# Kernel optimization log

Measured on AMD Instinct MI355X. Metric: run time of the kernel, lower is better.

Reference implementation:

```python
import jax, jax.numpy as jnp
import numpy as np

P, C_IN, C_OUT, V = 3, 64, 32, 8192
EPS = 1e-5


def _layernorm(z, w, b):
    # normalized_shape = [C, 1, V]: normalize jointly over channel/temporal/node dims
    m = jnp.mean(z, axis=(1, 2, 3), keepdims=True)
    v = jnp.var(z, axis=(1, 2, 3), keepdims=True)
    return (z - m) * jax.lax.rsqrt(v + EPS) * w + b


def setup_inputs() -> dict:
    key = jax.random.key(0)
    ks = jax.random.split(key, 8)
    return {
        "x": jax.random.normal(ks[0], (1, C_IN, 1, V), jnp.float32),
        "A": jax.random.uniform(ks[1], (P, V, V), jnp.float32),
        "conv_w": jax.random.normal(ks[2], (C_OUT * P, C_IN), jnp.float32) * 0.1,
        "conv_b": jax.random.normal(ks[3], (C_OUT * P,), jnp.float32) * 0.1,
        "fifo_front": jax.random.normal(ks[4], (1, C_OUT, 1, V), jnp.float32),
        "acc_slot": jax.random.normal(ks[5], (1, C_OUT, 1, V), jnp.float32),
        "ln_w": jnp.ones((C_OUT, 1, V), jnp.float32),
        "ln_b": jnp.zeros((C_OUT, 1, V), jnp.float32),
        "res_w": jax.random.normal(ks[6], (C_OUT, C_IN), jnp.float32) * 0.1,
        "res_ln_w": jnp.ones((C_OUT, 1, V), jnp.float32),
        "res_ln_b": jnp.zeros((C_OUT, 1, V), jnp.float32),
    }


def reference(x, A, conv_w, conv_b, fifo_front, acc_slot, ln_w, ln_b, res_w, res_ln_w, res_ln_b):
    # residual branch: 1x1 conv (no bias) + LayerNorm
    res = _layernorm(jnp.einsum('oc,nclv->nolv', res_w, x), res_ln_w, res_ln_b)

    # main branch: 1x1 conv to P*C_out channels
    h = jnp.einsum('oc,nclv->nolv', conv_w, x) + conv_b[None, :, None, None]  # (1, P*C, 1, V)
    h = h.reshape(P, C_OUT, V)  # split into P partition chunks of C_OUT channels (N=1, L=1)

    # per-partition graph aggregation, summed over partitions
    y = jnp.einsum('pcv,pvw->cw', h, A)[None, :, None, :]  # (1, C, 1, V)

    # FIFO/accumulator step at fresh indices: acc += y; acc -= fifo_front; output = acc slot
    agg = acc_slot + y - fifo_front

    out = jax.nn.relu(_layernorm(agg, ln_w, ln_b))
    out = jax.nn.relu(out + res)  # residual add, then ReLU (Dropout is identity at inference)
    return out
```

## Files before the change

### kernel.cpp

```cpp
#include <hip/hip_runtime.h>
#include <hip/hip_bf16.h>


#define PP 3
#define CIN 64
#define COUT 32
#define VV 8192
#define EPSL 1e-5f

typedef short v8s __attribute__((ext_vector_type(8)));
typedef float v4f __attribute__((ext_vector_type(4)));

__device__ __forceinline__ void block_reduce2_atomic(float s1, float s2,
                                                     float* d1, float* d2) {
  #pragma unroll
  for (int off = 32; off > 0; off >>= 1) {
    s1 += __shfl_down(s1, off, 64);
    s2 += __shfl_down(s2, off, 64);
  }
  __shared__ float r1[4], r2[4];
  int lane = threadIdx.x & 63, wv = threadIdx.x >> 6;
  if (lane == 0) { r1[wv] = s1; r2[wv] = s2; }
  __syncthreads();
  if (threadIdx.x == 0) {
    atomicAdd(d1, r1[0] + r1[1] + r1[2] + r1[3]);
    atomicAdd(d2, r2[0] + r2[1] + r2[2] + r2[3]);
  }
}

__global__ __launch_bounds__(256) void k1_conv(
    const float* __restrict__ x, const float* __restrict__ conv_w,
    const float* __restrict__ conv_b, const float* __restrict__ res_w,
    __hip_bfloat16* __restrict__ h, float* __restrict__ res,
    float* __restrict__ stats) {
  int v = blockIdx.x * 256 + threadIdx.x;
  int og = blockIdx.y;
  float xr[CIN];
  #pragma unroll
  for (int c = 0; c < CIN; ++c) xr[c] = x[c * VV + v];

  if (og < 3) {
    for (int i = 0; i < 32; ++i) {
      int o = og * 32 + i;
      float acc = conv_b[o];
      #pragma unroll
      for (int c = 0; c < CIN; ++c) acc = fmaf(conv_w[o * CIN + c], xr[c], acc);
      h[o * VV + v] = __float2bfloat16(acc);
    }
  } else {
    float s1 = 0.f, s2 = 0.f;
    for (int o = 0; o < COUT; ++o) {
      float acc = 0.f;
      #pragma unroll
      for (int c = 0; c < CIN; ++c) acc = fmaf(res_w[o * CIN + c], xr[c], acc);
      res[o * VV + v] = acc;
      s1 += acc; s2 += acc * acc;
    }
    block_reduce2_atomic(s1, s2, &stats[0], &stats[1]);
  }
}

#define TN 128
#define KC 32
#define CHUNKS 48
#define PAIR_DW 260
#define PAIR_BYTES 1040
#define BUF_BYTES (16 * PAIR_BYTES)

__global__ __launch_bounds__(256) void k2_gemm(
    const float* __restrict__ A, const __hip_bfloat16* __restrict__ h,
    float* __restrict__ y) {
  __shared__ char lds_raw[2][BUF_BYTES];
  const int tid = threadIdx.x;
  const int wv = tid >> 6, lane = tid & 63;
  const int quad = lane >> 4, l15 = lane & 15;
  const int wbase = blockIdx.x * TN;
  const int kbase = blockIdx.y * (KC * CHUNKS);
  const int srow = lane >> 5;
  const int scol = (lane & 31) * 4;

  v4f acc[2][2] = {};

  auto stage = [&](int buf, int chunk) {
    int k0 = kbase + chunk * KC;
    int p = k0 >> 13, v0 = k0 & (VV - 1);
    const float* Ap = A + ((size_t)p << 26);
    for (int pr = wv; pr < 16; pr += 4) {
      const float* gp = Ap + (size_t)(v0 + 2 * pr + srow) * VV + wbase + scol;
      void* lp = (void*)&lds_raw[buf][pr * PAIR_BYTES];
      __builtin_amdgcn_global_load_lds(
          (const __attribute__((address_space(1))) void*)gp,
          (__attribute__((address_space(3))) void*)lp, 16, 0, 0);
    }
  };

  stage(0, 0);
  __syncthreads();

  for (int c = 0; c < CHUNKS; ++c) {
    int cur = c & 1;
    if (c + 1 < CHUNKS) stage(cur ^ 1, c + 1);

    int kk = kbase + c * KC;
    int p = kk >> 13, v0 = kk & (VV - 1);
    const float* lf = (const float*)lds_raw[cur];

    const __hip_bfloat16* hp =
        h + (size_t)(p * COUT + l15) * VV + v0 + quad * 8;
    v8s afrag0 = *(const v8s*)hp;
    v8s afrag1 = *(const v8s*)(hp + 16 * VV);

    #pragma unroll
    for (int nt = 0; nt < 2; ++nt) {
      int wl = wv * 32 + nt * 16 + l15;
      union { unsigned u[4]; v8s s; } bf;
      #pragma unroll
      for (int t = 0; t < 4; ++t) {
        int pr = quad * 4 + t;
        float f0 = lf[pr * PAIR_DW + wl];
        float f1 = lf[pr * PAIR_DW + 128 + wl];
        bf.u[t] = __builtin_amdgcn_perm(__float_as_uint(f1),
                                        __float_as_uint(f0), 0x07060302u);
      }
      acc[0][nt] = __builtin_amdgcn_mfma_f32_16x16x32_bf16(afrag0, bf.s, acc[0][nt], 0, 0, 0);
      acc[1][nt] = __builtin_amdgcn_mfma_f32_16x16x32_bf16(afrag1, bf.s, acc[1][nt], 0, 0, 0);
    }
    __syncthreads();
  }

  #pragma unroll
  for (int mt = 0; mt < 2; ++mt)
    #pragma unroll
    for (int nt = 0; nt < 2; ++nt)
      #pragma unroll
      for (int r = 0; r < 4; ++r) {
        int crow = mt * 16 + quad * 4 + r;
        int w = wbase + wv * 32 + nt * 16 + l15;
        atomicAdd(&y[(size_t)crow * VV + w], acc[mt][nt][r]);
      }
}

__global__ __launch_bounds__(256) void k3_agg(
    const float* __restrict__ acc_slot, const float* __restrict__ fifo,
    float* __restrict__ y, float* __restrict__ stats) {
  int i = blockIdx.x * 256 + threadIdx.x;
  float4 yv = ((const float4*)y)[i];
  float4 av = ((const float4*)acc_slot)[i];
  float4 fv = ((const float4*)fifo)[i];
  float4 g;
  g.x = av.x + yv.x - fv.x;
  g.y = av.y + yv.y - fv.y;
  g.z = av.z + yv.z - fv.z;
  g.w = av.w + yv.w - fv.w;
  ((float4*)y)[i] = g;
  float s1 = g.x + g.y + g.z + g.w;
  float s2 = g.x * g.x + g.y * g.y + g.z * g.z + g.w * g.w;
  block_reduce2_atomic(s1, s2, &stats[2], &stats[3]);
}

__global__ __launch_bounds__(256) void k4_final(
    const float* __restrict__ agg, const float* __restrict__ res,
    const float* __restrict__ ln_w, const float* __restrict__ ln_b,
    const float* __restrict__ res_ln_w, const float* __restrict__ res_ln_b,
    const float* __restrict__ stats, float* __restrict__ out) {
  const float inv_n = 1.0f / (COUT * VV);
  float mr = stats[0] * inv_n;
  float vr = stats[1] * inv_n - mr * mr;
  float rsr = rsqrtf(vr + EPSL);
  float ma = stats[2] * inv_n;
  float va = stats[3] * inv_n - ma * ma;
  float rsa = rsqrtf(va + EPSL);

  int i = blockIdx.x * 256 + threadIdx.x;
  float4 g = ((const float4*)agg)[i];
  float4 r = ((const float4*)res)[i];
  float4 w1 = ((const float4*)ln_w)[i], b1 = ((const float4*)ln_b)[i];
  float4 w2 = ((const float4*)res_ln_w)[i], b2 = ((const float4*)res_ln_b)[i];
  float4 o;
  o.x = fmaxf(fmaxf((g.x - ma) * rsa * w1.x + b1.x, 0.f) + (r.x - mr) * rsr * w2.x + b2.x, 0.f);
  o.y = fmaxf(fmaxf((g.y - ma) * rsa * w1.y + b1.y, 0.f) + (r.y - mr) * rsr * w2.y + b2.y, 0.f);
  o.z = fmaxf(fmaxf((g.z - ma) * rsa * w1.z + b1.z, 0.f) + (r.z - mr) * rsr * w2.z + b2.z, 0.f);
  o.w = fmaxf(fmaxf((g.w - ma) * rsa * w1.w + b1.w, 0.f) + (r.w - mr) * rsr * w2.w + b2.w, 0.f);
  ((float4*)out)[i] = o;
}

extern "C" void kernel_launch(void* const* d_in, const int* in_sizes, int n_in,
                              void* d_out, int out_size, void* d_ws, size_t ws_size,
                              hipStream_t stream) {
  const float* x        = (const float*)d_in[0];
  const float* A        = (const float*)d_in[1];
  const float* conv_w   = (const float*)d_in[2];
  const float* conv_b   = (const float*)d_in[3];
  const float* fifo     = (const float*)d_in[4];
  const float* acc_slot = (const float*)d_in[5];
  const float* ln_w     = (const float*)d_in[6];
  const float* ln_b     = (const float*)d_in[7];
  const float* res_w    = (const float*)d_in[8];
  const float* res_ln_w = (const float*)d_in[9];
  const float* res_ln_b = (const float*)d_in[10];
  float* out = (float*)d_out;

  char* ws = (char*)d_ws;
  __hip_bfloat16* h = (__hip_bfloat16*)ws;
  float* y     = (float*)(ws + 1572864);
  float* res   = (float*)(ws + 1572864 + 1048576);
  float* stats = (float*)(ws + 1572864 + 2097152);

  hipMemsetAsync(y, 0, COUT * VV * sizeof(float), stream);
  hipMemsetAsync(stats, 0, 4 * sizeof(float), stream);

  k1_conv<<<dim3(32, 4), 256, 0, stream>>>(x, conv_w, conv_b, res_w, h, res, stats);
  k2_gemm<<<dim3(VV / TN, 16), 256, 0, stream>>>(A, h, y);
  k3_agg<<<256, 256, 0, stream>>>(acc_slot, fifo, y, stats);
  k4_final<<<256, 256, 0, stream>>>(y, res, ln_w, ln_b, res_ln_w, res_ln_b, stats, out);
}
```

Measured before the change: 1.050 ms.

## Triple-buffer GEMM staging and replace atomics with split-K partial buffers

The GEMM now keeps three LDS stages and prefetches the next h fragments into registers. It waits with an explicit vmcnt and a raw barrier instead of a full __syncthreads, which lets more loads overlap. Split-K results go to per-slice partial buffers that the aggregation kernel sums, and the LayerNorm statistics use per-block partials reduced in the final kernel. This removes the two memsets and all float atomics, at the cost of roughly 16 MB of extra partial writes and reads.

```diff
diff --git a/kernel.cpp b/kernel.cpp
--- a/kernel.cpp
+++ b/kernel.cpp
@@ -7,12 +7,13 @@
 #define COUT 32
 #define VV 8192
 #define EPSL 1e-5f
+#define SPLITK 16
 
 typedef short v8s __attribute__((ext_vector_type(8)));
 typedef float v4f __attribute__((ext_vector_type(4)));
 
-__device__ __forceinline__ void block_reduce2_atomic(float s1, float s2,
-                                                     float* d1, float* d2) {
+__device__ __forceinline__ void block_reduce2_store(float s1, float s2,
+                                                    float* dst) {
   #pragma unroll
   for (int off = 32; off > 0; off >>= 1) {
     s1 += __shfl_down(s1, off, 64);
@@ -23,8 +24,8 @@
   if (lane == 0) { r1[wv] = s1; r2[wv] = s2; }
   __syncthreads();
   if (threadIdx.x == 0) {
-    atomicAdd(d1, r1[0] + r1[1] + r1[2] + r1[3]);
-    atomicAdd(d2, r2[0] + r2[1] + r2[2] + r2[3]);
+    dst[0] = r1[0] + r1[1] + r1[2] + r1[3];
+    dst[1] = r2[0] + r2[1] + r2[2] + r2[3];
   }
 }
 
@@ -32,7 +33,7 @@
     const float* __restrict__ x, const float* __restrict__ conv_w,
     const float* __restrict__ conv_b, const float* __restrict__ res_w,
     __hip_bfloat16* __restrict__ h, float* __restrict__ res,
-    float* __restrict__ stats) {
+    float* __restrict__ res_part) {
   int v = blockIdx.x * 256 + threadIdx.x;
   int og = blockIdx.y;
   float xr[CIN];
@@ -56,7 +57,7 @@
       res[o * VV + v] = acc;
       s1 += acc; s2 += acc * acc;
     }
-    block_reduce2_atomic(s1, s2, &stats[0], &stats[1]);
+    block_reduce2_store(s1, s2, &res_part[blockIdx.x * 2]);
   }
 }
 
@@ -69,8 +70,8 @@
 
 __global__ __launch_bounds__(256) void k2_gemm(
     const float* __restrict__ A, const __hip_bfloat16* __restrict__ h,
-    float* __restrict__ y) {
-  __shared__ char lds_raw[2][BUF_BYTES];
+    float* __restrict__ y_part) {
+  __shared__ char lds_raw[3][BUF_BYTES];
   const int tid = threadIdx.x;
   const int wv = tid >> 6, lane = tid & 63;
   const int quad = lane >> 4, l15 = lane & 15;
@@ -81,53 +82,67 @@
 
   v4f acc[2][2] = {};
 
-  auto stage = [&](int buf, int chunk) {
+  auto stage = [&](char* buf, int chunk) {
     int k0 = kbase + chunk * KC;
     int p = k0 >> 13, v0 = k0 & (VV - 1);
     const float* Ap = A + ((size_t)p << 26);
     for (int pr = wv; pr < 16; pr += 4) {
       const float* gp = Ap + (size_t)(v0 + 2 * pr + srow) * VV + wbase + scol;
-      void* lp = (void*)&lds_raw[buf][pr * PAIR_BYTES];
+      void* lp = (void*)(buf + pr * PAIR_BYTES);
       __builtin_amdgcn_global_load_lds(
           (const __attribute__((address_space(1))) void*)gp,
           (__attribute__((address_space(3))) void*)lp, 16, 0, 0);
     }
   };
 
-  stage(0, 0);
-  __syncthreads();
-
-  for (int c = 0; c < CHUNKS; ++c) {
-    int cur = c & 1;
-    if (c + 1 < CHUNKS) stage(cur ^ 1, c + 1);
-
-    int kk = kbase + c * KC;
-    int p = kk >> 13, v0 = kk & (VV - 1);
-    const float* lf = (const float*)lds_raw[cur];
-
-    const __hip_bfloat16* hp =
-        h + (size_t)(p * COUT + l15) * VV + v0 + quad * 8;
-    v8s afrag0 = *(const v8s*)hp;
-    v8s afrag1 = *(const v8s*)(hp + 16 * VV);
-
-    #pragma unroll
-    for (int nt = 0; nt < 2; ++nt) {
-      int wl = wv * 32 + nt * 16 + l15;
-      union { unsigned u[4]; v8s s; } bf;
-      #pragma unroll
-      for (int t = 0; t < 4; ++t) {
-        int pr = quad * 4 + t;
-        float f0 = lf[pr * PAIR_DW + wl];
-        float f1 = lf[pr * PAIR_DW + 128 + wl];
-        bf.u[t] = __builtin_amdgcn_perm(__float_as_uint(f1),
-                                        __float_as_uint(f0), 0x07060302u);
+  {
+    int p0 = kbase >> 13, v00 = kbase & (VV - 1);
+    const __hip_bfloat16* hp0 = h + (size_t)(p0 * COUT + l15) * VV + v00 + quad * 8;
+    v8s tmp0 = *(const v8s*)hp0;
+    v8s tmp1 = *(const v8s*)(hp0 + 16 * VV);
+    stage(lds_raw[0], 0);
+
+    v8s hfr0 = tmp0, hfr1 = tmp1;
+
+    for (int c = 0; c < CHUNKS; ++c) {
+      v8s hn0 = hfr0, hn1 = hfr1;
+      if (c + 1 < CHUNKS) {
+        int kk = kbase + (c + 1) * KC;
+        int p = kk >> 13, v0n = kk & (VV - 1);
+        const __hip_bfloat16* hpn =
+            h + (size_t)(p * COUT + l15) * VV + v0n + quad * 8;
+        hn0 = *(const v8s*)hpn;
+        hn1 = *(const v8s*)(hpn + 16 * VV);
+        stage(lds_raw[(c + 1) % 3], c + 1);
+        asm volatile("s_waitcnt vmcnt(6)" ::: "memory");
+      } else {
+        asm volatile("s_waitcnt vmcnt(0)" ::: "memory");
       }
-      acc[0][nt] = __builtin_amdgcn_mfma_f32_16x16x32_bf16(afrag0, bf.s, acc[0][nt], 0, 0, 0);
-      acc[1][nt] = __builtin_amdgcn_mfma_f32_16x16x32_bf16(afrag1, bf.s, acc[1][nt], 0, 0, 0);
-    }
-    __syncthreads();
-  }
-
+      __builtin_amdgcn_s_barrier();
+      asm volatile("" ::: "memory");
+
+      const float* lf = (const float*)lds_raw[c % 3];
+
+      #pragma unroll
+      for (int nt = 0; nt < 2; ++nt) {
+        int wl = wv * 32 + nt * 16 + l15;
+        union { unsigned u[4]; v8s s; } bf;
+        #pragma unroll
+        for (int t = 0; t < 4; ++t) {
+          int pr = quad * 4 + t;
+          float f0 = lf[pr * PAIR_DW + wl];
+          float f1 = lf[pr * PAIR_DW + 128 + wl];
+          bf.u[t] = __builtin_amdgcn_perm(__float_as_uint(f1),
+                                          __float_as_uint(f0), 0x07060302u);
+        }
+        acc[0][nt] = __builtin_amdgcn_mfma_f32_16x16x32_bf16(hfr0, bf.s, acc[0][nt], 0, 0, 0);
+        acc[1][nt] = __builtin_amdgcn_mfma_f32_16x16x32_bf16(hfr1, bf.s, acc[1][nt], 0, 0, 0);
+      }
+      hfr0 = hn0; hfr1 = hn1;
+    }
+  }
+
+  float* yp = y_part + (size_t)blockIdx.y * COUT * VV;
   #pragma unroll
   for (int mt = 0; mt < 2; ++mt)
     #pragma unroll
@@ -136,40 +151,70 @@
       for (int r = 0; r < 4; ++r) {
         int crow = mt * 16 + quad * 4 + r;
         int w = wbase + wv * 32 + nt * 16 + l15;
-        atomicAdd(&y[(size_t)crow * VV + w], acc[mt][nt][r]);
+        yp[(size_t)crow * VV + w] = acc[mt][nt][r];
       }
 }
 
 __global__ __launch_bounds__(256) void k3_agg(
     const float* __restrict__ acc_slot, const float* __restrict__ fifo,
-    float* __restrict__ y, float* __restrict__ stats) {
+    const float* __restrict__ y_part, float* __restrict__ agg,
+    float* __restrict__ agg_part) {
   int i = blockIdx.x * 256 + threadIdx.x;
-  float4 yv = ((const float4*)y)[i];
+  float4 s = ((const float4*)y_part)[i];
+  #pragma unroll
+  for (int kb = 1; kb < SPLITK; ++kb) {
+    float4 t = ((const float4*)(y_part + (size_t)kb * COUT * VV))[i];
+    s.x += t.x; s.y += t.y; s.z += t.z; s.w += t.w;
+  }
   float4 av = ((const float4*)acc_slot)[i];
   float4 fv = ((const float4*)fifo)[i];
   float4 g;
-  g.x = av.x + yv.x - fv.x;
-  g.y = av.y + yv.y - fv.y;
-  g.z = av.z + yv.z - fv.z;
-  g.w = av.w + yv.w - fv.w;
-  ((float4*)y)[i] = g;
+  g.x = av.x + s.x - fv.x;
+  g.y = av.y + s.y - fv.y;
+  g.z = av.z + s.z - fv.z;
+  g.w = av.w + s.w - fv.w;
+  ((float4*)agg)[i] = g;
   float s1 = g.x + g.y + g.z + g.w;
   float s2 = g.x * g.x + g.y * g.y + g.z * g.z + g.w * g.w;
-  block_reduce2_atomic(s1, s2, &stats[2], &stats[3]);
+  block_reduce2_store(s1, s2, &agg_part[blockIdx.x * 2]);
 }
 
 __global__ __launch_bounds__(256) void k4_final(
     const float* __restrict__ agg, const float* __restrict__ res,
     const float* __restrict__ ln_w, const float* __restrict__ ln_b,
     const float* __restrict__ res_ln_w, const float* __restrict__ res_ln_b,
-    const float* __restrict__ stats, float* __restrict__ out) {
-  const float inv_n = 1.0f / (COUT * VV);
-  float mr = stats[0] * inv_n;
-  float vr = stats[1] * inv_n - mr * mr;
-  float rsr = rsqrtf(vr + EPSL);
-  float ma = stats[2] * inv_n;
-  float va = stats[3] * inv_n - ma * ma;
-  float rsa = rsqrtf(va + EPSL);
+    const float* __restrict__ res_part, const float* __restrict__ agg_part,
+    float* __restrict__ out) {
+  __shared__ float sf[4];
+  if (threadIdx.x < 64) {
+    int lane = threadIdx.x;
+    float a1 = 0.f, a2 = 0.f;
+    #pragma unroll
+    for (int j = 0; j < 4; ++j) {
+      a1 += agg_part[2 * (lane + 64 * j)];
+      a2 += agg_part[2 * (lane + 64 * j) + 1];
+    }
+    float r1 = 0.f, r2 = 0.f;
+    if (lane < 32) { r1 = res_part[2 * lane]; r2 = res_part[2 * lane + 1]; }
+    #pragma unroll
+    for (int off = 32; off > 0; off >>= 1) {
+      a1 += __shfl_down(a1, off, 64);
+      a2 += __shfl_down(a2, off, 64);
+      r1 += __shfl_down(r1, off, 64);
+      r2 += __shfl_down(r2, off, 64);
+    }
+    if (lane == 0) {
+      const float inv_n = 1.0f / (COUT * VV);
+      float mr = r1 * inv_n;
+      float vr = r2 * inv_n - mr * mr;
+      float ma = a1 * inv_n;
+      float va = a2 * inv_n - ma * ma;
+      sf[0] = mr; sf[1] = rsqrtf(vr + EPSL);
+      sf[2] = ma; sf[3] = rsqrtf(va + EPSL);
+    }
+  }
+  __syncthreads();
+  const float mr = sf[0], rsr = sf[1], ma = sf[2], rsa = sf[3];
 
   int i = blockIdx.x * 256 + threadIdx.x;
   float4 g = ((const float4*)agg)[i];
@@ -201,16 +246,16 @@
   float* out = (float*)d_out;
 
   char* ws = (char*)d_ws;
-  __hip_bfloat16* h = (__hip_bfloat16*)ws;
-  float* y     = (float*)(ws + 1572864);
-  float* res   = (float*)(ws + 1572864 + 1048576);
-  float* stats = (float*)(ws + 1572864 + 2097152);
-
-  hipMemsetAsync(y, 0, COUT * VV * sizeof(float), stream);
-  hipMemsetAsync(stats, 0, 4 * sizeof(float), stream);
-
-  k1_conv<<<dim3(32, 4), 256, 0, stream>>>(x, conv_w, conv_b, res_w, h, res, stats);
-  k2_gemm<<<dim3(VV / TN, 16), 256, 0, stream>>>(A, h, y);
-  k3_agg<<<256, 256, 0, stream>>>(acc_slot, fifo, y, stats);
-  k4_final<<<256, 256, 0, stream>>>(y, res, ln_w, ln_b, res_ln_w, res_ln_b, stats, out);
-}
+  __hip_bfloat16* h  = (__hip_bfloat16*)ws;
+  float* y_part   = (float*)(ws + 1572864);
+  float* agg      = (float*)(ws + 18350080);
+  float* res      = (float*)(ws + 19398656);
+  float* res_part = (float*)(ws + 20447232);
+  float* agg_part = (float*)(ws + 20447488);
+
+  k1_conv<<<dim3(32, 4), 256, 0, stream>>>(x, conv_w, conv_b, res_w, h, res, res_part);
+  k2_gemm<<<dim3(VV / TN, SPLITK), 256, 0, stream>>>(A, h, y_part);
+  k3_agg<<<256, 256, 0, stream>>>(acc_slot, fifo, y_part, agg, agg_part);
+  k4_final<<<256, 256, 0, stream>>>(agg, res, ln_w, ln_b, res_ln_w, res_ln_b,
+                                    res_part, agg_part, out);
+}
```

New measurement: 1.046 ms. About the same (-0.4%).
